# Kernel optimization log

Hardware: AMD Instinct MI355X
Metric: run time of the kernel (lower is better)

Reference implementation:

```python
import jax, jax.numpy as jnp
import numpy as np

C = 128   # channels
C4 = C // 4

def setup_inputs() -> dict:
    key = jax.random.key(0)
    k1, k2, k3, k4, k5 = jax.random.split(key, 5)
    B, N = 16, 2048
    x_h = jax.random.normal(k1, (B, C, N), dtype=jnp.float32)
    x_o = jax.random.normal(k2, (B, C, N), dtype=jnp.float32)
    # q_conv and k_conv share the SAME weight (tied in __init__), bias=False
    w_qk = jax.random.normal(k3, (C4, C), dtype=jnp.float32) * (1.0 / np.sqrt(C))
    # v_conv: Conv1d(C, C, 1) with bias
    w_v = jax.random.normal(k4, (C, C), dtype=jnp.float32) * (1.0 / np.sqrt(C))
    b_v = jax.random.normal(k5, (C,), dtype=jnp.float32) * 0.01
    return {"x_h": x_h, "x_o": x_o, "w_qk": w_qk, "w_v": w_v, "b_v": b_v}

def reference(x_h, x_o, w_qk, w_v, b_v):
    # SA_Layer_1 forward (only layer used by Grasp_Transformer_Last.forward)
    # 1x1 conv == channel matmul
    xh_q = jnp.einsum('dc,bcn->bnd', w_qk, x_h)            # [B, Nh, C4]
    xo_k = jnp.einsum('dc,bcm->bdm', w_qk, x_o)            # [B, C4, No]
    alpha = jnp.einsum('bnd,bdm->bnm', xh_q, xo_k)         # [B, Nh, No]
    # no softmax: normalize by column sums over dim=1 (Nh axis)
    attention = alpha / (1e-9 + jnp.sum(alpha, axis=1, keepdims=True))
    xo_v = jnp.einsum('dc,bcm->bmd', w_v, x_o) + b_v       # [B, No, C]
    x_r = jnp.einsum('bnm,bmd->bnd', attention, xo_v)      # [B, Nh, C]
    x_r = jnp.transpose(x_r, (0, 2, 1))                    # [B, C, Nh]
    return (x_r, attention)
```

## Files before the change

kernel.cpp:

```cpp
#include <hip/hip_runtime.h>

constexpr int NTOK = 2048;
constexpr int CH   = 128;
constexpr int C4   = 32;
constexpr int NB   = 16;

typedef __attribute__((ext_vector_type(8))) __bf16 bf16x8;
typedef __attribute__((ext_vector_type(4))) float  f32x4;

__device__ __forceinline__ unsigned short f2bf(float f) {
  union { float f; unsigned u; } v; v.f = f;
  unsigned r = v.u + 0x7fffu + ((v.u >> 16) & 1u);
  return (unsigned short)(r >> 16);
}
__device__ __forceinline__ float bf2f(unsigned short h) {
  union { unsigned u; float f; } v; v.u = ((unsigned)h) << 16;
  return v.f;
}

__global__ __launch_bounds__(256) void rs_kernel(const float* __restrict__ x_h,
                                                 double* __restrict__ rowsumH) {
  const int lane = threadIdx.x & 63;
  const int c = blockIdx.x * 4 + (threadIdx.x >> 6);
  const int b = blockIdx.y;
  const float* rp = x_h + (size_t)(b * CH + c) * NTOK;
  double s = 0.0;
#pragma unroll
  for (int i = 0; i < 8; ++i) {
    float4 v = *(const float4*)(rp + (lane + 64 * i) * 4);
    s += (double)v.x + (double)v.y + (double)v.z + (double)v.w;
  }
  for (int off = 1; off <= 32; off <<= 1) s += __shfl_xor(s, off);
  if (lane == 0) rowsumH[b * CH + c] = s;
}

__global__ __launch_bounds__(256) void prep_qk(const float* __restrict__ x_h,
                                               const float* __restrict__ x_o,
                                               const float* __restrict__ w_qk,
                                               const double* __restrict__ rowsumH,
                                               float* __restrict__ xhq_f32,
                                               float* __restrict__ xokT_f32,
                                               unsigned short* __restrict__ xhq_hi,
                                               unsigned short* __restrict__ xokT_hi,
                                               unsigned short* __restrict__ xhq_lo,
                                               unsigned short* __restrict__ xokT_lo,
                                               float* __restrict__ inv) {
  const int t = threadIdx.x;
  const int n0 = blockIdx.x * 64;
  const int b = blockIdx.y;
  const int which = blockIdx.z;
  const float* src = which ? x_o : x_h;
  float* dstf = which ? xokT_f32 : xhq_f32;
  unsigned short* dsth = which ? xokT_hi : xhq_hi;
  unsigned short* dstl = which ? xokT_lo : xhq_lo;

  __shared__ float Xt[CH][64];
  __shared__ float Wl[C4][132];
  __shared__ double Sl[C4];
  __shared__ double Pl[CH];

  for (int i = 0; i < 8; ++i) {
    int flat = t + 256 * i;
    int c = flat >> 4, f4 = flat & 15;
    float4 v = *(const float4*)(src + (size_t)(b * CH + c) * NTOK + n0 + f4 * 4);
    *(float4*)&Xt[c][f4 * 4] = v;
  }
  for (int i = 0; i < 4; ++i) {
    int flat = t + 256 * i;
    int d = flat >> 5, f4 = flat & 31;
    float4 v = *(const float4*)(w_qk + d * CH + f4 * 4);
    *(float4*)&Wl[d][f4 * 4] = v;
  }
  __syncthreads();

  const int nb = (t & 15) * 4;
  const int d0 = (t >> 4) * 2;
  float acc[4][2] = {};
#pragma unroll 4
  for (int c = 0; c < CH; ++c) {
    float4 x4 = *(const float4*)&Xt[c][nb];
    float w0 = Wl[d0][c], w1 = Wl[d0 + 1][c];
    acc[0][0] += x4.x * w0; acc[0][1] += x4.x * w1;
    acc[1][0] += x4.y * w0; acc[1][1] += x4.y * w1;
    acc[2][0] += x4.z * w0; acc[2][1] += x4.z * w1;
    acc[3][0] += x4.w * w0; acc[3][1] += x4.w * w1;
  }

  const size_t robase = (size_t)(b * NTOK + n0 + nb);
#pragma unroll
  for (int i = 0; i < 4; ++i) {
    size_t base = (robase + i) * C4 + d0;
    *(float2*)(dstf + base) = make_float2(acc[i][0], acc[i][1]);
    unsigned short h0 = f2bf(acc[i][0]), h1 = f2bf(acc[i][1]);
    *(unsigned*)(dsth + base) = (unsigned)h0 | ((unsigned)h1 << 16);
    unsigned short l0 = f2bf(acc[i][0] - bf2f(h0));
    unsigned short l1 = f2bf(acc[i][1] - bf2f(h1));
    *(unsigned*)(dstl + base) = (unsigned)l0 | ((unsigned)l1 << 16);
  }

  if (which) {
    if (t < C4) {
      double s = 0.0;
      for (int c = 0; c < CH; ++c) s += (double)Wl[t][c] * rowsumH[b * CH + c];
      Sl[t] = s;
    }
    __syncthreads();
    if (t < CH) {
      double p = 0.0;
      for (int d = 0; d < C4; ++d) p += Sl[d] * (double)Wl[d][t];
      Pl[t] = p;
    }
    __syncthreads();
    if (t < 64) {
      double s = 0.0;
      for (int c = 0; c < CH; ++c) s += Pl[c] * (double)Xt[c][t];
      inv[b * NTOK + n0 + t] = (float)(1.0 / (1e-9 + s));
    }
  }
}

__global__ __launch_bounds__(256) void u_kernel(const float* __restrict__ x_o,
                                                const float* __restrict__ xokT_f32,
                                                const float* __restrict__ inv,
                                                float* __restrict__ U4) {
  const int t = threadIdx.x;
  const int c0 = blockIdx.x * 8;
  const int slab = blockIdx.y;
  const int mbase0 = slab * 512;
  const int b = blockIdx.z;
  const int d = t & 31, cl = t >> 5;
  __shared__ float Xs[8][256];
  float acc = 0.f;
  for (int cc = 0; cc < 2; ++cc) {
    const int mb = mbase0 + cc * 256;
    __syncthreads();
    for (int i = 0; i < 2; ++i) {
      int flat = t + 256 * i;
      int row = flat >> 6, f4 = flat & 63;
      float4 xv = *(const float4*)(x_o + (size_t)(b * CH + c0 + row) * NTOK + mb + f4 * 4);
      float4 iv = *(const float4*)(inv + b * NTOK + mb + f4 * 4);
      xv.x *= iv.x; xv.y *= iv.y; xv.z *= iv.z; xv.w *= iv.w;
      *(float4*)&Xs[row][f4 * 4] = xv;
    }
    __syncthreads();
    const float* ap = xokT_f32 + (size_t)(b * NTOK + mb) * C4 + d;
#pragma unroll 4
    for (int mm = 0; mm < 256; mm += 4) {
      float4 xq = *(const float4*)&Xs[cl][mm];
      float a0 = ap[(mm + 0) * C4];
      float a1 = ap[(mm + 1) * C4];
      float a2 = ap[(mm + 2) * C4];
      float a3 = ap[(mm + 3) * C4];
      acc += a0 * xq.x + a1 * xq.y + a2 * xq.z + a3 * xq.w;
    }
  }
  U4[(size_t)((b * 4 + slab) * C4 + d) * CH + c0 + cl] = acc;
}

__global__ __launch_bounds__(256) void t_kernel(const float* __restrict__ U4,
                                                const float* __restrict__ w_v,
                                                const float* __restrict__ b_v,
                                                const float* __restrict__ xokT_f32,
                                                const float* __restrict__ inv,
                                                float* __restrict__ T) {
  const int t = threadIdx.x, b = blockIdx.x;
  __shared__ float Wl[CH * CH];
  __shared__ float S2s[8][C4];
  const int d = t & 31;
  const int g = t >> 5;
  {
    const float* kp = xokT_f32 + (size_t)b * NTOK * C4;
    const float* ip = inv + b * NTOK;
    float s = 0.f;
    for (int m = g * 256; m < g * 256 + 256; ++m) s += kp[(size_t)m * C4 + d] * ip[m];
    S2s[g][d] = s;
  }
  for (int i = 0; i < 16; ++i) {
    int flat = t + 256 * i;
    *(float4*)&Wl[flat * 4] = *(const float4*)(w_v + flat * 4);
  }
  __syncthreads();
  float s2 = 0.f;
#pragma unroll
  for (int gg = 0; gg < 8; ++gg) s2 += S2s[gg][d];
  const int cg = g * 16;
  float acc[16] = {};
  const float* up = U4 + (size_t)(b * 4 * C4 + d) * CH;
  for (int cp = 0; cp < CH; ++cp) {
    float u = up[cp] + up[C4 * CH + cp] + up[2 * C4 * CH + cp] + up[3 * C4 * CH + cp];
#pragma unroll
    for (int j = 0; j < 16; ++j) acc[j] += u * Wl[(cg + j) * CH + cp];
  }
#pragma unroll
  for (int j = 0; j < 16; ++j) acc[j] += s2 * b_v[cg + j];
  float* tp = T + (size_t)(b * C4 + d) * CH + cg;
#pragma unroll
  for (int j = 0; j < 16; j += 4)
    *(float4*)(tp + j) = make_float4(acc[j], acc[j + 1], acc[j + 2], acc[j + 3]);
}

__global__ __launch_bounds__(256) void xr_kernel(const float* __restrict__ xhq_f32,
                                                 const float* __restrict__ T,
                                                 float* __restrict__ out0) {
  const int t = threadIdx.x;
  const int n = blockIdx.x * 256 + t;
  const int b = blockIdx.y;
  __shared__ float Tl[CH][36];
  for (int i = 0; i < 16; ++i) {
    int flat = t + 256 * i;
    int d = flat >> 7, c = flat & 127;
    Tl[c][d] = T[(size_t)b * C4 * CH + flat];
  }
  __syncthreads();
  float xq[C4];
  const float* qp = xhq_f32 + (size_t)(b * NTOK + n) * C4;
#pragma unroll
  for (int i = 0; i < 8; ++i) {
    float4 v = *(const float4*)(qp + i * 4);
    xq[i * 4] = v.x; xq[i * 4 + 1] = v.y; xq[i * 4 + 2] = v.z; xq[i * 4 + 3] = v.w;
  }
  float* op = out0 + (size_t)b * CH * NTOK + n;
  for (int c = 0; c < CH; ++c) {
    float acc = 0.f;
#pragma unroll
    for (int dd = 0; dd < C4; dd += 4) {
      float4 tv = *(const float4*)&Tl[c][dd];
      acc += xq[dd] * tv.x + xq[dd + 1] * tv.y + xq[dd + 2] * tv.z + xq[dd + 3] * tv.w;
    }
    op[(size_t)c * NTOK] = acc;
  }
}

__global__ __launch_bounds__(256) void attn_kernel(const unsigned short* __restrict__ xhq_hi,
                                                   const unsigned short* __restrict__ xhq_lo,
                                                   const unsigned short* __restrict__ xokT_hi,
                                                   const unsigned short* __restrict__ xokT_lo,
                                                   const float* __restrict__ inv,
                                                   float* __restrict__ out1) {
  const int t = threadIdx.x;
  const int wave = t >> 6, lane = t & 63;
  const int quad = lane >> 4, l16 = lane & 15;
  const int m0 = blockIdx.x * 64;
  const int n0 = blockIdx.y * 64;
  const int b = blockIdx.z;

  const int n = n0 + wave * 16 + l16;
  const size_t abase = (size_t)(b * NTOK + n) * C4 + quad * 8;
  bf16x8 ah = *(const bf16x8*)(const void*)(xhq_hi + abase);
  bf16x8 al = *(const bf16x8*)(const void*)(xhq_lo + abase);

  bf16x8 bh[4], bl[4];
  float invv[4];
#pragma unroll
  for (int tt = 0; tt < 4; ++tt) {
    int m = m0 + tt * 16 + l16;
    size_t bbase = (size_t)(b * NTOK + m) * C4 + quad * 8;
    bh[tt] = *(const bf16x8*)(const void*)(xokT_hi + bbase);
    bl[tt] = *(const bf16x8*)(const void*)(xokT_lo + bbase);
    invv[tt] = inv[b * NTOK + m];
  }

  const int nrow = n0 + wave * 16 + quad * 4;
#pragma unroll
  for (int tt = 0; tt < 4; ++tt) {
    f32x4 z = {0.f, 0.f, 0.f, 0.f};
    f32x4 acc = __builtin_amdgcn_mfma_f32_16x16x32_bf16(al, bh[tt], z, 0, 0, 0);
    acc = __builtin_amdgcn_mfma_f32_16x16x32_bf16(ah, bl[tt], acc, 0, 0, 0);
    acc = __builtin_amdgcn_mfma_f32_16x16x32_bf16(ah, bh[tt], acc, 0, 0, 0);
#pragma unroll
    for (int r = 0; r < 4; ++r) {
      float v = acc[r] * invv[tt];
      size_t off = ((size_t)(b * NTOK) + nrow + r) * NTOK + m0 + tt * 16 + l16;
      __builtin_nontemporal_store(v, out1 + off);
    }
  }
}

extern "C" void kernel_launch(void* const* d_in, const int* in_sizes, int n_in,
                              void* d_out, int out_size, void* d_ws, size_t ws_size,
                              hipStream_t stream) {
  (void)in_sizes; (void)n_in; (void)out_size; (void)ws_size;
  const float* x_h  = (const float*)d_in[0];
  const float* x_o  = (const float*)d_in[1];
  const float* w_qk = (const float*)d_in[2];
  const float* w_v  = (const float*)d_in[3];
  const float* b_v  = (const float*)d_in[4];
  float* out0 = (float*)d_out;
  float* out1 = out0 + (size_t)NB * CH * NTOK;

  char* ws = (char*)d_ws;
  float* xhq_f32        = (float*)(ws + 0);
  float* xokT_f32       = (float*)(ws + 4194304);
  unsigned short* xhq_hi  = (unsigned short*)(ws + 8388608);
  unsigned short* xokT_hi = (unsigned short*)(ws + 10485760);
  unsigned short* xhq_lo  = (unsigned short*)(ws + 12582912);
  unsigned short* xokT_lo = (unsigned short*)(ws + 14680064);
  float* inv      = (float*)(ws + 16777216);
  float* U4       = (float*)(ws + 16908288);
  float* T        = (float*)(ws + 17956864);
  double* rowsumH = (double*)(ws + 18219008);

  rs_kernel <<<dim3(32, NB), 256, 0, stream>>>(x_h, rowsumH);
  prep_qk   <<<dim3(32, NB, 2), 256, 0, stream>>>(x_h, x_o, w_qk, rowsumH,
                                                  xhq_f32, xokT_f32,
                                                  xhq_hi, xokT_hi, xhq_lo, xokT_lo, inv);
  u_kernel  <<<dim3(16, 4, NB), 256, 0, stream>>>(x_o, xokT_f32, inv, U4);
  t_kernel  <<<NB, 256, 0, stream>>>(U4, w_v, b_v, xokT_f32, inv, T);
  xr_kernel <<<dim3(8, NB), 256, 0, stream>>>(xhq_f32, T, out0);
  attn_kernel<<<dim3(32, 32, NB), 256, 0, stream>>>(xhq_hi, xhq_lo, xokT_hi, xokT_lo,
                                                    inv, out1);
}
```

Measured before the change: 427.1 us.

## Stage attention tile in LDS for vector stores and widen small kernels' grids

The attention kernel now writes its normalized 64x64 tile into shared memory and then emits coalesced 16-byte nontemporal row stores, replacing scattered scalar stores. The t_kernel is split across channel groups so it launches 128 blocks instead of 16, and xr_kernel splits channels across four thread groups with more blocks. This targets store efficiency on the large attention output and low occupancy in the small kernels, at the cost of extra LDS use and a barrier.

```diff
diff --git a/kernel.cpp b/kernel.cpp
--- a/kernel.cpp
+++ b/kernel.cpp
@@ -163,11 +163,13 @@
                                                 const float* __restrict__ xokT_f32,
                                                 const float* __restrict__ inv,
                                                 float* __restrict__ T) {
-  const int t = threadIdx.x, b = blockIdx.x;
-  __shared__ float Wl[CH * CH];
-  __shared__ float S2s[8][C4];
+  const int t = threadIdx.x;
+  const int cgrp = blockIdx.x;
+  const int b = blockIdx.y;
   const int d = t & 31;
   const int g = t >> 5;
+  __shared__ float Wl[16][CH];
+  __shared__ float S2s[8][C4];
   {
     const float* kp = xokT_f32 + (size_t)b * NTOK * C4;
     const float* ip = inv + b * NTOK;
@@ -175,39 +177,39 @@
     for (int m = g * 256; m < g * 256 + 256; ++m) s += kp[(size_t)m * C4 + d] * ip[m];
     S2s[g][d] = s;
   }
-  for (int i = 0; i < 16; ++i) {
+  for (int i = 0; i < 2; ++i) {
     int flat = t + 256 * i;
-    *(float4*)&Wl[flat * 4] = *(const float4*)(w_v + flat * 4);
+    *(float4*)&Wl[0][flat * 4] = *(const float4*)(w_v + (size_t)cgrp * 16 * CH + flat * 4);
   }
   __syncthreads();
   float s2 = 0.f;
 #pragma unroll
   for (int gg = 0; gg < 8; ++gg) s2 += S2s[gg][d];
-  const int cg = g * 16;
-  float acc[16] = {};
+  const int c0 = g * 2;
+  float acc0 = 0.f, acc1 = 0.f;
   const float* up = U4 + (size_t)(b * 4 * C4 + d) * CH;
   for (int cp = 0; cp < CH; ++cp) {
     float u = up[cp] + up[C4 * CH + cp] + up[2 * C4 * CH + cp] + up[3 * C4 * CH + cp];
-#pragma unroll
-    for (int j = 0; j < 16; ++j) acc[j] += u * Wl[(cg + j) * CH + cp];
-  }
-#pragma unroll
-  for (int j = 0; j < 16; ++j) acc[j] += s2 * b_v[cg + j];
-  float* tp = T + (size_t)(b * C4 + d) * CH + cg;
-#pragma unroll
-  for (int j = 0; j < 16; j += 4)
-    *(float4*)(tp + j) = make_float4(acc[j], acc[j + 1], acc[j + 2], acc[j + 3]);
-}
-
-__global__ __launch_bounds__(256) void xr_kernel(const float* __restrict__ xhq_f32,
+    acc0 += u * Wl[c0][cp];
+    acc1 += u * Wl[c0 + 1][cp];
+  }
+  const int cglob = cgrp * 16 + c0;
+  acc0 += s2 * b_v[cglob];
+  acc1 += s2 * b_v[cglob + 1];
+  *(float2*)(T + (size_t)(b * C4 + d) * CH + cglob) = make_float2(acc0, acc1);
+}
+
+__global__ __launch_bounds__(512) void xr_kernel(const float* __restrict__ xhq_f32,
                                                  const float* __restrict__ T,
                                                  float* __restrict__ out0) {
   const int t = threadIdx.x;
-  const int n = blockIdx.x * 256 + t;
+  const int nl = t & 127;
+  const int half = t >> 7;
+  const int n = blockIdx.x * 128 + nl;
   const int b = blockIdx.y;
   __shared__ float Tl[CH][36];
-  for (int i = 0; i < 16; ++i) {
-    int flat = t + 256 * i;
+  for (int i = 0; i < 8; ++i) {
+    int flat = t + 512 * i;
     int d = flat >> 7, c = flat & 127;
     Tl[c][d] = T[(size_t)b * C4 * CH + flat];
   }
@@ -220,7 +222,7 @@
     xq[i * 4] = v.x; xq[i * 4 + 1] = v.y; xq[i * 4 + 2] = v.z; xq[i * 4 + 3] = v.w;
   }
   float* op = out0 + (size_t)b * CH * NTOK + n;
-  for (int c = 0; c < CH; ++c) {
+  for (int c = half * 32; c < half * 32 + 32; ++c) {
     float acc = 0.f;
 #pragma unroll
     for (int dd = 0; dd < C4; dd += 4) {
@@ -244,6 +246,8 @@
   const int n0 = blockIdx.y * 64;
   const int b = blockIdx.z;
 
+  __shared__ float tile[64][68];
+
   const int n = n0 + wave * 16 + l16;
   const size_t abase = (size_t)(b * NTOK + n) * C4 + quad * 8;
   bf16x8 ah = *(const bf16x8*)(const void*)(xhq_hi + abase);
@@ -260,7 +264,7 @@
     invv[tt] = inv[b * NTOK + m];
   }
 
-  const int nrow = n0 + wave * 16 + quad * 4;
+  const int trow = wave * 16 + quad * 4;
 #pragma unroll
   for (int tt = 0; tt < 4; ++tt) {
     f32x4 z = {0.f, 0.f, 0.f, 0.f};
@@ -268,11 +272,18 @@
     acc = __builtin_amdgcn_mfma_f32_16x16x32_bf16(ah, bl[tt], acc, 0, 0, 0);
     acc = __builtin_amdgcn_mfma_f32_16x16x32_bf16(ah, bh[tt], acc, 0, 0, 0);
 #pragma unroll
-    for (int r = 0; r < 4; ++r) {
-      float v = acc[r] * invv[tt];
-      size_t off = ((size_t)(b * NTOK) + nrow + r) * NTOK + m0 + tt * 16 + l16;
-      __builtin_nontemporal_store(v, out1 + off);
-    }
+    for (int r = 0; r < 4; ++r)
+      tile[trow + r][tt * 16 + l16] = acc[r] * invv[tt];
+  }
+  __syncthreads();
+
+  const int g = lane >> 4;
+#pragma unroll
+  for (int s = 0; s < 4; ++s) {
+    const int row = wave * 4 + g + s * 16;
+    f32x4 v = *(const f32x4*)&tile[row][l16 * 4];
+    float* dst = out1 + ((size_t)(b * NTOK) + n0 + row) * NTOK + m0 + l16 * 4;
+    __builtin_nontemporal_store(v, (f32x4*)dst);
   }
 }
 
@@ -305,8 +316,8 @@
                                                   xhq_f32, xokT_f32,
                                                   xhq_hi, xokT_hi, xhq_lo, xokT_lo, inv);
   u_kernel  <<<dim3(16, 4, NB), 256, 0, stream>>>(x_o, xokT_f32, inv, U4);
-  t_kernel  <<<NB, 256, 0, stream>>>(U4, w_v, b_v, xokT_f32, inv, T);
-  xr_kernel <<<dim3(8, NB), 256, 0, stream>>>(xhq_f32, T, out0);
+  t_kernel  <<<dim3(8, NB), 256, 0, stream>>>(U4, w_v, b_v, xokT_f32, inv, T);
+  xr_kernel <<<dim3(16, NB), 512, 0, stream>>>(xhq_f32, T, out0);
   attn_kernel<<<dim3(32, 32, NB), 256, 0, stream>>>(xhq_hi, xhq_lo, xokT_hi, xokT_lo,
                                                     inv, out1);
 }
```

Result: faster. 387.1 us (-9.4%).
